# Kernel tuning notes

Hardware: AMD Instinct MI355X
Metric: run time of the kernel (lower is better)

## Reference

```python
import jax, jax.numpy as jnp
import numpy as np

DMODEL = 1024
NHEAD = 16
DHEAD = DMODEL // NHEAD

def _layernorm(x, g, b, eps=1e-5):
    mu = jnp.mean(x, axis=-1, keepdims=True)
    var = jnp.var(x, axis=-1, keepdims=True)
    return (x - mu) * jax.lax.rsqrt(var + eps) * g + b

def setup_inputs() -> dict:
    key = jax.random.key(0)
    ks = jax.random.split(key, 12)
    b, lq, lv, d = 2, 2048, 2048, DMODEL
    s = 1.0 / np.sqrt(d)
    return {
        "q": jax.random.normal(ks[0], (b, lq, d), jnp.float32),
        "k": jax.random.normal(ks[1], (b, lv, d), jnp.float32),
        "v": jax.random.normal(ks[2], (b, lv, d), jnp.float32),
        "qln_g": jnp.ones((d,), jnp.float32),
        "qln_b": jnp.zeros((d,), jnp.float32),
        "kvln_g": jnp.ones((d,), jnp.float32),
        "kvln_b": jnp.zeros((d,), jnp.float32),
        "Wq": jax.random.normal(ks[3], (d, d), jnp.float32) * s,
        "Wk": jax.random.normal(ks[4], (d, d), jnp.float32) * s,
        "Wv": jax.random.normal(ks[5], (d, d), jnp.float32) * s,
        "Wg": jax.random.normal(ks[6], (d, d), jnp.float32) * s,
        "bg": jnp.zeros((d,), jnp.float32),
        "Wo": jax.random.normal(ks[7], (d, d), jnp.float32) * s,
    }

def reference(q, k, v, qln_g, qln_b, kvln_g, kvln_b, Wq, Wk, Wv, Wg, bg, Wo):
    b, lq, d = q.shape
    lv = v.shape[1]
    qn = _layernorm(q, qln_g, qln_b)           # [b, lq, d]
    q_ = qn @ Wq.T
    kk = _layernorm(k, kvln_g, kvln_b) @ Wk.T
    vv = _layernorm(v, kvln_g, kvln_b) @ Wv.T
    qh = q_.reshape(b, lq, NHEAD, DHEAD)       # bqhd
    kh = kk.reshape(b, lv, NHEAD, DHEAD)
    vh = vv.reshape(b, lv, NHEAD, DHEAD)
    scores = jnp.einsum('bqhd,bkhd->bhqk', qh, kh) / np.sqrt(DHEAD)
    attn = jax.nn.softmax(scores, axis=-1)
    y = jnp.einsum('bhqk,bkhd->bqhd', attn, vh).reshape(b, lq, d)
    g = jax.nn.sigmoid(qn @ Wg.T + bg)
    return (y * g) @ Wo.T
```

## Files before the change

### kernel.cpp

```cpp
#include <hip/hip_runtime.h>
#include <hip/hip_bf16.h>

#define DMODEL 1024
#define NHEAD  16
#define DHEAD  64
#define BATCH  2
#define LQ     2048
#define LV     2048
#define ROWS   (BATCH*LQ)
#define WELEMS (DMODEL*DMODEL)
#define BH     (BATCH*NHEAD)

typedef short bf16x8 __attribute__((ext_vector_type(8)));
typedef float f32x4  __attribute__((ext_vector_type(4)));

__device__ __forceinline__ float bf2f(unsigned short s) {
    union { unsigned u; float f; } v; v.u = ((unsigned)s) << 16;
    return v.f;
}
__device__ __forceinline__ unsigned pk_bf(float a, float b) {
    union { __hip_bfloat162 h; unsigned u; } c;
    c.h = __float22bfloat162_rn(make_float2(a, b));
    return c.u;
}

__device__ __forceinline__ void cp16_g2l(const void* g, void* l) {
    __builtin_amdgcn_global_load_lds(
        (const __attribute__((address_space(1))) void*)g,
        (__attribute__((address_space(3))) void*)l,
        16, 0, 0);
}

#define QSCALE (0.125f * 1.4426950408889634f)

#define PREP_WBLK (5 * 256)
#define PREP_NBLK (PREP_WBLK + 3 * ROWS / 4)

__global__ __launch_bounds__(256) void prep_kernel(
    const float* q, const float* k, const float* v,
    const float* qg, const float* qb, const float* kvg, const float* kvb,
    const float* Wq, const float* Wk, const float* Wv, const float* Wg, const float* Wo,
    unsigned short* qn, unsigned short* kn, unsigned short* vn, unsigned short* wb)
{
    int bx = blockIdx.x, tid = threadIdx.x;
    if (bx < PREP_WBLK) {
        int z = bx >> 8;
        const float* srcs[5] = {Wq, Wk, Wv, Wg, Wo};
        size_t base = (size_t)(bx & 255) * 4096;
        const float* s = srcs[z] + base;
        unsigned short* d = wb + (size_t)z * WELEMS + base;
        #pragma unroll
        for (int u = 0; u < 4; ++u) {
            int i = u * 1024 + tid * 4;
            float4 x = *(const float4*)(s + i);
            *(uint2*)(d + i) = make_uint2(pk_bf(x.x, x.y), pk_bf(x.z, x.w));
        }
        return;
    }
    int wave = tid >> 6, lane = tid & 63;
    int gr = (bx - PREP_WBLK) * 4 + wave;
    int tz = gr >> 12, row = gr & 4095;
    const float *x, *gp, *bp; unsigned short* o;
    if      (tz == 0) { x = q; gp = qg;  bp = qb;  o = qn; }
    else if (tz == 1) { x = k; gp = kvg; bp = kvb; o = kn; }
    else              { x = v; gp = kvg; bp = kvb; o = vn; }
    const float* xr = x + (size_t)row * DMODEL;

    float4 xv[4];
    float s = 0.f, sq = 0.f;
    #pragma unroll
    for (int u = 0; u < 4; ++u) {
        xv[u] = *(const float4*)(xr + u * 256 + lane * 4);
        s  += xv[u].x + xv[u].y + xv[u].z + xv[u].w;
        sq += xv[u].x*xv[u].x + xv[u].y*xv[u].y + xv[u].z*xv[u].z + xv[u].w*xv[u].w;
    }
    #pragma unroll
    for (int off = 1; off < 64; off <<= 1) { s += __shfl_xor(s, off); sq += __shfl_xor(sq, off); }
    float mu  = s * (1.0f / DMODEL);
    float var = sq * (1.0f / DMODEL) - mu * mu;
    float inv = rsqrtf(var + 1e-5f);

    unsigned short* orow = o + (size_t)row * DMODEL;
    #pragma unroll
    for (int u = 0; u < 4; ++u) {
        int col = u * 256 + lane * 4;
        float4 gv = *(const float4*)(gp + col);
        float4 bv = *(const float4*)(bp + col);
        float r0 = (xv[u].x - mu) * inv * gv.x + bv.x;
        float r1 = (xv[u].y - mu) * inv * gv.y + bv.y;
        float r2 = (xv[u].z - mu) * inv * gv.z + bv.z;
        float r3 = (xv[u].w - mu) * inv * gv.w + bv.w;
        *(uint2*)(orow + col) = make_uint2(pk_bf(r0, r1), pk_bf(r2, r3));
    }
}

template<int MODE>
__device__ __forceinline__ void gemm256_core(
    const unsigned short* A, const unsigned short* Bw,
    unsigned short* Obf, const float* bias, float scale,
    unsigned short* Al, unsigned short* Bl, int bm, int bn)
{
    int tid  = threadIdx.x;
    int w = tid >> 6, l = tid & 63, quad = l >> 4, L = l & 15;
    int wm = w >> 2, wn = w & 3;

    int c16 = (l & 7) ^ (l >> 3);
    const unsigned short* gAs = A  + (size_t)(bm * 256 + w * 8 + (l >> 3)) * DMODEL + c16 * 8;
    const unsigned short* gBs = Bw + (size_t)(bn * 256 + w * 8 + (l >> 3)) * DMODEL + c16 * 8;
    int dstE = w * 512;

    #define STG_A2(t, ro) do { const unsigned short* s_ = gAs + (size_t)(ro) * DMODEL + (t) * 64; \
        unsigned short* d_ = Al + ((t) & 1) * 16384 + (ro) * 64 + dstE;                           \
        cp16_g2l(s_, d_); cp16_g2l(s_ + 64 * DMODEL, d_ + 4096); } while (0)
    #define STG_B2(t, ro) do { const unsigned short* s_ = gBs + (size_t)(ro) * DMODEL + (t) * 64; \
        unsigned short* d_ = Bl + ((t) & 1) * 16384 + (ro) * 64 + dstE;                           \
        cp16_g2l(s_, d_); cp16_g2l(s_ + 64 * DMODEL, d_ + 4096); } while (0)

    int sw = (L & 7) << 3;
    int o0 = (quad * 8) ^ sw;
    int o1 = (32 + quad * 8) ^ sw;

    f32x4 acc[8][4];
    #pragma unroll
    for (int i = 0; i < 8; ++i)
        #pragma unroll
        for (int j = 0; j < 4; ++j) acc[i][j] = (f32x4){0.f, 0.f, 0.f, 0.f};

    STG_A2(0, 0); STG_A2(0, 128); STG_B2(0, 0); STG_B2(0, 128);
    STG_A2(1, 0); STG_A2(1, 128);
    asm volatile("s_waitcnt vmcnt(4)" ::: "memory");
    __builtin_amdgcn_s_barrier();

    const int NT = DMODEL / 64;
    for (int t = 0; t < NT; ++t) {
        const unsigned short* Ab = Al + (t & 1) * 16384 + wm * 8192;
        const unsigned short* Bb = Bl + (t & 1) * 16384 + wn * 4096;
        bf16x8 b0[4], b1[4], a0[2], a1[2], r0v[6], r1v[6];

        #pragma unroll
        for (int j = 0; j < 4; ++j) {
            b0[j] = *(const bf16x8*)&Bb[(j * 16 + L) * 64 + o0];
            b1[j] = *(const bf16x8*)&Bb[(j * 16 + L) * 64 + o1];
        }
        #pragma unroll
        for (int i2 = 0; i2 < 2; ++i2) {
            a0[i2] = *(const bf16x8*)&Ab[(i2 * 16 + L) * 64 + o0];
            a1[i2] = *(const bf16x8*)&Ab[(i2 * 16 + L) * 64 + o1];
        }
        if (t + 1 < NT) STG_B2(t + 1, 0);
        __builtin_amdgcn_s_barrier();
        __builtin_amdgcn_s_setprio(1);
        #pragma unroll
        for (int i2 = 0; i2 < 2; ++i2)
            #pragma unroll
            for (int j = 0; j < 4; ++j) {
                if (MODE == 3) {
                    acc[i2][j] = __builtin_amdgcn_mfma_f32_16x16x32_bf16(a0[i2], b0[j], acc[i2][j], 0, 0, 0);
                    acc[i2][j] = __builtin_amdgcn_mfma_f32_16x16x32_bf16(a1[i2], b1[j], acc[i2][j], 0, 0, 0);
                } else {
                    acc[i2][j] = __builtin_amdgcn_mfma_f32_16x16x32_bf16(b0[j], a0[i2], acc[i2][j], 0, 0, 0);
                    acc[i2][j] = __builtin_amdgcn_mfma_f32_16x16x32_bf16(b1[j], a1[i2], acc[i2][j], 0, 0, 0);
                }
            }
        __builtin_amdgcn_s_setprio(0);
        __builtin_amdgcn_s_barrier();

        #pragma unroll
        for (int r = 0; r < 6; ++r) {
            r0v[r] = *(const bf16x8*)&Ab[((32 + r * 16) + L) * 64 + o0];
            r1v[r] = *(const bf16x8*)&Ab[((32 + r * 16) + L) * 64 + o1];
        }
        if (t + 1 < NT) STG_B2(t + 1, 128);
        __builtin_amdgcn_s_barrier();
        __builtin_amdgcn_s_setprio(1);
        #pragma unroll
        for (int i2 = 0; i2 < 2; ++i2)
            #pragma unroll
            for (int j = 0; j < 4; ++j) {
                if (MODE == 3) {
                    acc[2 + i2][j] = __builtin_amdgcn_mfma_f32_16x16x32_bf16(r0v[i2], b0[j], acc[2 + i2][j], 0, 0, 0);
                    acc[2 + i2][j] = __builtin_amdgcn_mfma_f32_16x16x32_bf16(r1v[i2], b1[j], acc[2 + i2][j], 0, 0, 0);
                } else {
                    acc[2 + i2][j] = __builtin_amdgcn_mfma_f32_16x16x32_bf16(b0[j], r0v[i2], acc[2 + i2][j], 0, 0, 0);
                    acc[2 + i2][j] = __builtin_amdgcn_mfma_f32_16x16x32_bf16(b1[j], r1v[i2], acc[2 + i2][j], 0, 0, 0);
                }
            }
        __builtin_amdgcn_s_setprio(0);
        asm volatile("s_waitcnt lgkmcnt(0)" ::: "memory");
        __builtin_amdgcn_sched_barrier(0);
        __builtin_amdgcn_s_barrier();

        if (t + 2 < NT) { STG_A2(t + 2, 0); STG_A2(t + 2, 128); }
        __builtin_amdgcn_s_barrier();
        __builtin_amdgcn_s_setprio(1);
        #pragma unroll
        for (int i2 = 0; i2 < 4; ++i2)
            #pragma unroll
            for (int j = 0; j < 4; ++j) {
                if (MODE == 3) {
                    acc[4 + i2][j] = __builtin_amdgcn_mfma_f32_16x16x32_bf16(r0v[2 + i2], b0[j], acc[4 + i2][j], 0, 0, 0);
                    acc[4 + i2][j] = __builtin_amdgcn_mfma_f32_16x16x32_bf16(r1v[2 + i2], b1[j], acc[4 + i2][j], 0, 0, 0);
                } else {
                    acc[4 + i2][j] = __builtin_amdgcn_mfma_f32_16x16x32_bf16(b0[j], r0v[2 + i2], acc[4 + i2][j], 0, 0, 0);
                    acc[4 + i2][j] = __builtin_amdgcn_mfma_f32_16x16x32_bf16(b1[j], r1v[2 + i2], acc[4 + i2][j], 0, 0, 0);
                }
            }
        __builtin_amdgcn_s_setprio(0);
        if (t + 2 < NT) asm volatile("s_waitcnt vmcnt(4)" ::: "memory");
        else            asm volatile("s_waitcnt vmcnt(0)" ::: "memory");
        __builtin_amdgcn_s_barrier();
    }
    #undef STG_A2
    #undef STG_B2

    #pragma unroll
    for (int i = 0; i < 8; ++i) {
        #pragma unroll
        for (int j = 0; j < 4; ++j) {
            f32x4 a = acc[i][j];
            if (MODE == 3) {
                int gcol  = bn * 256 + wn * 64 + j * 16 + L;
                int grow0 = bm * 256 + wm * 128 + i * 16 + quad * 4;
                int b = grow0 >> 11, key0 = grow0 & 2047;
                int h = gcol >> 6,   dd   = gcol & 63;
                uint2 o = make_uint2(pk_bf(a[0], a[1]), pk_bf(a[2], a[3]));
                *(uint2*)&Obf[(((size_t)(b * NHEAD + h) * DHEAD + dd) << 11) + key0] = o;
            } else {
                int grow  = bm * 256 + wm * 128 + i * 16 + L;
                int gcol0 = bn * 256 + wn * 64 + j * 16 + quad * 4;
                size_t idx = (size_t)grow * DMODEL + gcol0;
                if (MODE == 0) {
                    uint2 o = make_uint2(pk_bf(a[0] * scale, a[1] * scale),
                                         pk_bf(a[2] * scale, a[3] * scale));
                    *(uint2*)&Obf[idx] = o;
                } else {
                    float4 bv = *(const float4*)&bias[gcol0];
                    float s0 = 1.0f / (1.0f + __expf(-(a[0] + bv.x)));
                    float s1 = 1.0f / (1.0f + __expf(-(a[1] + bv.y)));
                    float s2 = 1.0f / (1.0f + __expf(-(a[2] + bv.z)));
                    float s3 = 1.0f / (1.0f + __expf(-(a[3] + bv.w)));
                    *(uint2*)&Obf[idx] = make_uint2(pk_bf(s0, s1), pk_bf(s2, s3));
                }
            }
        }
    }
}

__global__ __launch_bounds__(512, 2) void gemm256_kernel(
    const unsigned short* qn, const unsigned short* kn, const unsigned short* vn,
    const unsigned short* wb,
    unsigned short* qs, unsigned short* kkp, unsigned short* vt, unsigned short* gate,
    const float* bg)
{
    __shared__ __align__(16) unsigned short Al[2 * 256 * 64];
    __shared__ __align__(16) unsigned short Bl[2 * 256 * 64];
    int f = blockIdx.x, xcd = f & 7, s = f >> 3;
    int z  = xcd & 3;
    int bm = ((xcd >> 2) << 3) | (s >> 2);
    int bn = s & 3;
    switch (z) {
        case 0:  gemm256_core<0>(qn, wb + 0 * WELEMS, qs,   nullptr, QSCALE, Al, Bl, bm, bn); break;
        case 1:  gemm256_core<0>(kn, wb + 1 * WELEMS, kkp,  nullptr, 1.0f,   Al, Bl, bm, bn); break;
        case 2:  gemm256_core<3>(vn, wb + 2 * WELEMS, vt,   nullptr, 1.0f,   Al, Bl, bm, bn); break;
        default: gemm256_core<1>(qn, wb + 3 * WELEMS, gate, bg,      1.0f,   Al, Bl, bm, bn); break;
    }
}

__device__ __forceinline__ void xcd_map(int& bm, int& bn) {
    int f = blockIdx.y * 8 + blockIdx.x;
    int xcd = f & 7, s = f >> 3;
    bn = s & 7;
    bm = ((s >> 3) << 3) | xcd;
}

__global__ __launch_bounds__(256, 2) void gemm_f32out_kernel(
    const unsigned short* A, const unsigned short* Bw, float* O)
{
    __shared__ __align__(16) unsigned short Al[2 * 128 * 64];
    __shared__ __align__(16) unsigned short Bl[2 * 128 * 64];
    int bm, bn; xcd_map(bm, bn);
    int tid = threadIdx.x;
    int w = tid >> 6, l = tid & 63, quad = l >> 4, L = l & 15;
    int wm = w >> 1, wn = w & 1;

    int c16 = (l & 7) ^ (l >> 3);
    const unsigned short* gAs = A  + (size_t)(bm * 128 + w * 8 + (l >> 3)) * DMODEL + c16 * 8;
    const unsigned short* gBs = Bw + (size_t)(bn * 128 + w * 8 + (l >> 3)) * DMODEL + c16 * 8;
    int dstE = w * 512;

    #define STG4(t, gp, lp) do { const unsigned short* s_ = (gp) + (t) * 64;  \
        unsigned short* d_ = (lp) + ((t) & 1) * 8192 + dstE;                  \
        cp16_g2l(s_,               d_);                                       \
        cp16_g2l(s_ + 32 * DMODEL, d_ + 2048);                                \
        cp16_g2l(s_ + 64 * DMODEL, d_ + 4096);                                \
        cp16_g2l(s_ + 96 * DMODEL, d_ + 6144); } while (0)

    int sw = (L & 7) << 3;
    int o0 = (quad * 8) ^ sw;
    int o1 = (32 + quad * 8) ^ sw;

    f32x4 acc[4][4];
    #pragma unroll
    for (int i = 0; i < 4; ++i)
        #pragma unroll
        for (int j = 0; j < 4; ++j) acc[i][j] = (f32x4){0.f, 0.f, 0.f, 0.f};

    STG4(0, gAs, Al); STG4(0, gBs, Bl);

    const int NT = DMODEL / 64;
    for (int t = 0; t < NT; ++t) {
        if (t + 1 < NT) {
            STG4(t + 1, gAs, Al); STG4(t + 1, gBs, Bl);
            asm volatile("s_waitcnt vmcnt(8)" ::: "memory");
        } else {
            asm volatile("s_waitcnt vmcnt(0)" ::: "memory");
        }
        __builtin_amdgcn_s_barrier();

        const unsigned short* Ab = Al + (t & 1) * 8192 + (wm * 64) * 64;
        const unsigned short* Bb = Bl + (t & 1) * 8192 + (wn * 64) * 64;
        bf16x8 a0[4], a1[4], b0[4], b1[4];
        #pragma unroll
        for (int j = 0; j < 4; ++j) {
            b0[j] = *(const bf16x8*)&Bb[(j * 16 + L) * 64 + o0];
            b1[j] = *(const bf16x8*)&Bb[(j * 16 + L) * 64 + o1];
        }
        #pragma unroll
        for (int i = 0; i < 4; ++i) {
            a0[i] = *(const bf16x8*)&Ab[(i * 16 + L) * 64 + o0];
            a1[i] = *(const bf16x8*)&Ab[(i * 16 + L) * 64 + o1];
        }
        __builtin_amdgcn_s_setprio(1);
        #pragma unroll
        for (int i = 0; i < 4; ++i)
            #pragma unroll
            for (int j = 0; j < 4; ++j) {
                acc[i][j] = __builtin_amdgcn_mfma_f32_16x16x32_bf16(b0[j], a0[i], acc[i][j], 0, 0, 0);
                acc[i][j] = __builtin_amdgcn_mfma_f32_16x16x32_bf16(b1[j], a1[i], acc[i][j], 0, 0, 0);
            }
        __builtin_amdgcn_s_setprio(0);
        __builtin_amdgcn_s_barrier();
    }
    #undef STG4

    #pragma unroll
    for (int i = 0; i < 4; ++i) {
        #pragma unroll
        for (int j = 0; j < 4; ++j) {
            int grow  = bm * 128 + wm * 64 + i * 16 + L;
            int gcol0 = bn * 128 + wn * 64 + j * 16 + quad * 4;
            *(f32x4*)&O[(size_t)grow * DMODEL + gcol0] = acc[i][j];
        }
    }
}

__global__ __launch_bounds__(256, 4) void attn_kernel(
    const unsigned short* qs, const unsigned short* kk, const unsigned short* vt,
    const unsigned short* gate, unsigned short* yg)
{
    __shared__ __align__(16) unsigned short Kl[2 * 64 * 64];
    __shared__ __align__(16) unsigned short Vl[3 * 64 * 64];

    int tid  = threadIdx.x;
    int wave = tid >> 6, lane = tid & 63, quad = lane >> 4, L = lane & 15;

    int f  = blockIdx.y * 32 + blockIdx.x;
    int bh = (f & 7) * 4 + ((f >> 3) & 3);
    int qt = f >> 5;
    int bb = bh >> 4, h = bh & 15;
    int q0 = qt * 64;

    const unsigned short* Qb =
        qs + ((size_t)(bb * LQ + q0 + wave * 16 + L)) * DMODEL + h * DHEAD;
    bf16x8 aq0 = *(const bf16x8*)(Qb + quad * 8);
    bf16x8 aq1 = *(const bf16x8*)(Qb + 32 + quad * 8);

    f32x4 acc[4];
    #pragma unroll
    for (int nt = 0; nt < 4; ++nt) acc[nt] = (f32x4){0.f, 0.f, 0.f, 0.f};
    f32x4 lacc = (f32x4){0.f, 0.f, 0.f, 0.f};
    bf16x8 ones;
    #pragma unroll
    for (int j = 0; j < 8; ++j) ones[j] = (short)0x3F80;

    int rloc = lane >> 3;
    int c16  = (lane & 7) ^ rloc;
    int key0 = (wave & 1) * 32 + (rloc >> 2) * 8 + (wave >> 1) * 4 + (rloc & 3);

    const unsigned short* gK = kk + (size_t)bb * LV * DMODEL + h * DHEAD
                                  + (size_t)key0 * DMODEL + c16 * 8;
    const unsigned short* gV = vt + ((size_t)((bb * NHEAD + h) * DHEAD
                                  + wave * 16 + rloc)) * LV + c16 * 8;
    char* KlB = (char*)Kl;
    char* VlB = (char*)Vl;
    int dst0 = wave * 2048;

    int sl0 = (quad ^ (L & 7)) * 8;

    cp16_g2l(gK,               KlB + dst0);
    cp16_g2l(gK + 16 * DMODEL, KlB + dst0 + 1024);
    cp16_g2l(gV,               VlB + dst0);
    cp16_g2l(gV + 8 * LV,      VlB + dst0 + 1024);
    __syncthreads();
    gK += 64 * DMODEL; gV += 64;
    cp16_g2l(gK,               KlB + 8192 + dst0);
    cp16_g2l(gK + 16 * DMODEL, KlB + 8192 + dst0 + 1024);
    cp16_g2l(gV,               VlB + 8192 + dst0);
    cp16_g2l(gV + 8 * LV,      VlB + 8192 + dst0 + 1024);

    bf16x8 pap0, pap1;

    {
        const unsigned short* Kb = Kl;
        f32x4 zz[4];
        __builtin_amdgcn_s_setprio(1);
        #pragma unroll
        for (int kt = 0; kt < 4; ++kt) {
            bf16x8 bk0 = *(const bf16x8*)&Kb[(kt * 16 + L) * 64 + sl0];
            bf16x8 bk1 = *(const bf16x8*)&Kb[(kt * 16 + L) * 64 + (sl0 ^ 32)];
            f32x4 z = (f32x4){0.f, 0.f, 0.f, 0.f};
            z = __builtin_amdgcn_mfma_f32_16x16x32_bf16(bk0, aq0, z, 0, 0, 0);
            z = __builtin_amdgcn_mfma_f32_16x16x32_bf16(bk1, aq1, z, 0, 0, 0);
            zz[kt] = z;
        }
        __builtin_amdgcn_s_setprio(0);
        union { unsigned u[4]; bf16x8 h; } pa0, pa1;
        pa0.u[0] = pk_bf(__builtin_amdgcn_exp2f(zz[0][0]), __builtin_amdgcn_exp2f(zz[0][1]));
        pa0.u[1] = pk_bf(__builtin_amdgcn_exp2f(zz[0][2]), __builtin_amdgcn_exp2f(zz[0][3]));
        pa0.u[2] = pk_bf(__builtin_amdgcn_exp2f(zz[2][0]), __builtin_amdgcn_exp2f(zz[2][1]));
        pa0.u[3] = pk_bf(__builtin_amdgcn_exp2f(zz[2][2]), __builtin_amdgcn_exp2f(zz[2][3]));
        pa1.u[0] = pk_bf(__builtin_amdgcn_exp2f(zz[1][0]), __builtin_amdgcn_exp2f(zz[1][1]));
        pa1.u[1] = pk_bf(__builtin_amdgcn_exp2f(zz[1][2]), __builtin_amdgcn_exp2f(zz[1][3]));
        pa1.u[2] = pk_bf(__builtin_amdgcn_exp2f(zz[3][0]), __builtin_amdgcn_exp2f(zz[3][1]));
        pa1.u[3] = pk_bf(__builtin_amdgcn_exp2f(zz[3][2]), __builtin_amdgcn_exp2f(zz[3][3]));
        pap0 = pa0.h; pap1 = pa1.h;
    }

    const int NT = LV / 64;
    int vs = 2;
    int vr = 0;
    for (int t = 1; t < NT; ++t) {
        __syncthreads();
        if (t + 1 < NT) {
            gK += 64 * DMODEL; gV += 64;
            int kb = ((t + 1) & 1) * 8192;
            cp16_g2l(gK,               KlB + kb + dst0);
            cp16_g2l(gK + 16 * DMODEL, KlB + kb + dst0 + 1024);
            int vb_ = vs * 8192;
            cp16_g2l(gV,               VlB + vb_ + dst0);
            cp16_g2l(gV + 8 * LV,      VlB + vb_ + dst0 + 1024);
            vs = (vs == 2) ? 0 : vs + 1;
        }
        const unsigned short* Vb = Vl + vr * 4096;
        vr = (vr == 2) ? 0 : vr + 1;
        const unsigned short* Kb = Kl + (t & 1) * 4096;

        bf16x8 vf0[4], vf1[4];
        #pragma unroll
        for (int nt = 0; nt < 4; ++nt) {
            vf0[nt] = *(const bf16x8*)&Vb[(nt * 16 + L) * 64 + sl0];
            vf1[nt] = *(const bf16x8*)&Vb[(nt * 16 + L) * 64 + (sl0 ^ 32)];
        }
        bf16x8 kf0[4], kf1[4];
        #pragma unroll
        for (int kt = 0; kt < 4; ++kt) {
            kf0[kt] = *(const bf16x8*)&Kb[(kt * 16 + L) * 64 + sl0];
            kf1[kt] = *(const bf16x8*)&Kb[(kt * 16 + L) * 64 + (sl0 ^ 32)];
        }

        __builtin_amdgcn_s_setprio(1);
        lacc = __builtin_amdgcn_mfma_f32_16x16x32_bf16(ones, pap0, lacc, 0, 0, 0);
        lacc = __builtin_amdgcn_mfma_f32_16x16x32_bf16(ones, pap1, lacc, 0, 0, 0);
        #pragma unroll
        for (int nt = 0; nt < 4; ++nt) {
            acc[nt] = __builtin_amdgcn_mfma_f32_16x16x32_bf16(vf0[nt], pap0, acc[nt], 0, 0, 0);
            acc[nt] = __builtin_amdgcn_mfma_f32_16x16x32_bf16(vf1[nt], pap1, acc[nt], 0, 0, 0);
        }
        f32x4 zz[4];
        #pragma unroll
        for (int kt = 0; kt < 4; ++kt) {
            f32x4 z = (f32x4){0.f, 0.f, 0.f, 0.f};
            z = __builtin_amdgcn_mfma_f32_16x16x32_bf16(kf0[kt], aq0, z, 0, 0, 0);
            z = __builtin_amdgcn_mfma_f32_16x16x32_bf16(kf1[kt], aq1, z, 0, 0, 0);
            zz[kt] = z;
        }
        __builtin_amdgcn_s_setprio(0);
        union { unsigned u[4]; bf16x8 h; } pa0, pa1;
        pa0.u[0] = pk_bf(__builtin_amdgcn_exp2f(zz[0][0]), __builtin_amdgcn_exp2f(zz[0][1]));
        pa0.u[1] = pk_bf(__builtin_amdgcn_exp2f(zz[0][2]), __builtin_amdgcn_exp2f(zz[0][3]));
        pa0.u[2] = pk_bf(__builtin_amdgcn_exp2f(zz[2][0]), __builtin_amdgcn_exp2f(zz[2][1]));
        pa0.u[3] = pk_bf(__builtin_amdgcn_exp2f(zz[2][2]), __builtin_amdgcn_exp2f(zz[2][3]));
        pa1.u[0] = pk_bf(__builtin_amdgcn_exp2f(zz[1][0]), __builtin_amdgcn_exp2f(zz[1][1]));
        pa1.u[1] = pk_bf(__builtin_amdgcn_exp2f(zz[1][2]), __builtin_amdgcn_exp2f(zz[1][3]));
        pa1.u[2] = pk_bf(__builtin_amdgcn_exp2f(zz[3][0]), __builtin_amdgcn_exp2f(zz[3][1]));
        pa1.u[3] = pk_bf(__builtin_amdgcn_exp2f(zz[3][2]), __builtin_amdgcn_exp2f(zz[3][3]));
        pap0 = pa0.h; pap1 = pa1.h;
    }

    {
        const unsigned short* Vb = Vl + 1 * 4096;
        bf16x8 vf0[4], vf1[4];
        #pragma unroll
        for (int nt = 0; nt < 4; ++nt) {
            vf0[nt] = *(const bf16x8*)&Vb[(nt * 16 + L) * 64 + sl0];
            vf1[nt] = *(const bf16x8*)&Vb[(nt * 16 + L) * 64 + (sl0 ^ 32)];
        }
        lacc = __builtin_amdgcn_mfma_f32_16x16x32_bf16(ones, pap0, lacc, 0, 0, 0);
        lacc = __builtin_amdgcn_mfma_f32_16x16x32_bf16(ones, pap1, lacc, 0, 0, 0);
        #pragma unroll
        for (int nt = 0; nt < 4; ++nt) {
            acc[nt] = __builtin_amdgcn_mfma_f32_16x16x32_bf16(vf0[nt], pap0, acc[nt], 0, 0, 0);
            acc[nt] = __builtin_amdgcn_mfma_f32_16x16x32_bf16(vf1[nt], pap1, acc[nt], 0, 0, 0);
        }
    }

    float inv_l = 1.0f / lacc[0];
    size_t rb = ((size_t)(bb * LQ + q0 + wave * 16 + L)) * DMODEL + h * DHEAD;
    #pragma unroll
    for (int nt = 0; nt < 4; ++nt) {
        size_t idx = rb + nt * 16 + quad * 4;
        ushort4 g = *(const ushort4*)&gate[idx];
        float y0 = acc[nt][0] * inv_l * bf2f(g.x);
        float y1 = acc[nt][1] * inv_l * bf2f(g.y);
        float y2 = acc[nt][2] * inv_l * bf2f(g.z);
        float y3 = acc[nt][3] * inv_l * bf2f(g.w);
        *(uint2*)&yg[idx] = make_uint2(pk_bf(y0, y1), pk_bf(y2, y3));
    }
}

extern "C" void kernel_launch(void* const* d_in, const int* in_sizes, int n_in,
                              void* d_out, int out_size, void* d_ws, size_t ws_size,
                              hipStream_t stream)
{
    const float* q      = (const float*)d_in[0];
    const float* k      = (const float*)d_in[1];
    const float* v      = (const float*)d_in[2];
    const float* qln_g  = (const float*)d_in[3];
    const float* qln_b  = (const float*)d_in[4];
    const float* kvln_g = (const float*)d_in[5];
    const float* kvln_b = (const float*)d_in[6];
    const float* Wq     = (const float*)d_in[7];
    const float* Wk     = (const float*)d_in[8];
    const float* Wv     = (const float*)d_in[9];
    const float* Wg     = (const float*)d_in[10];
    const float* bg     = (const float*)d_in[11];
    const float* Wo     = (const float*)d_in[12];
    float* out = (float*)d_out;

    const size_t T8 = (size_t)ROWS * DMODEL * 2;
    char* ws = (char*)d_ws;
    unsigned short* qn   = (unsigned short*)(ws + 0 * T8);
    unsigned short* kn   = (unsigned short*)(ws + 1 * T8);
    unsigned short* vn   = (unsigned short*)(ws + 2 * T8);
    unsigned short* qs   = (unsigned short*)(ws + 3 * T8);
    unsigned short* kkp  = (unsigned short*)(ws + 4 * T8);
    unsigned short* vt   = (unsigned short*)(ws + 5 * T8);
    unsigned short* gate = (unsigned short*)(ws + 6 * T8);
    unsigned short* yg   = (unsigned short*)(ws + 7 * T8);
    unsigned short* wb   = (unsigned short*)(ws + 8 * T8);

    prep_kernel<<<dim3(PREP_NBLK), 256, 0, stream>>>(
        q, k, v, qln_g, qln_b, kvln_g, kvln_b, Wq, Wk, Wv, Wg, Wo, qn, kn, vn, wb);
    gemm256_kernel<<<dim3(256), 512, 0, stream>>>(
        qn, kn, vn, wb, qs, kkp, vt, gate, bg);
    attn_kernel<<<dim3(32, 32), 256, 0, stream>>>(qs, kkp, vt, gate, yg);
    gemm_f32out_kernel<<<dim3(DMODEL / 128, ROWS / 128), 256, 0, stream>>>(yg, wb + 4 * WELEMS, out);
}
```

Measured before the change: 226.2 us.

## Restructure GEMM main loop into four phases with one-tile-ahead prefetch

Reorganizes the 256x256 bf16 GEMM core so each K-step runs in four MFMA phases, each loading only two A fragments, instead of three phases that preloaded six extra A fragments into registers. Global-to-LDS staging of the next tile is spread as single copies across the phases, and prefetch distance for A drops from two tiles ahead to one. The aim is to cut register pressure and interleave memory traffic more evenly with compute. The cost is more barriers per iteration and less latency hiding for A loads.

```diff
diff --git a/kernel.cpp b/kernel.cpp
--- a/kernel.cpp
+++ b/kernel.cpp
@@ -109,12 +109,9 @@
     const unsigned short* gBs = Bw + (size_t)(bn * 256 + w * 8 + (l >> 3)) * DMODEL + c16 * 8;
     int dstE = w * 512;
 
-    #define STG_A2(t, ro) do { const unsigned short* s_ = gAs + (size_t)(ro) * DMODEL + (t) * 64; \
-        unsigned short* d_ = Al + ((t) & 1) * 16384 + (ro) * 64 + dstE;                           \
-        cp16_g2l(s_, d_); cp16_g2l(s_ + 64 * DMODEL, d_ + 4096); } while (0)
-    #define STG_B2(t, ro) do { const unsigned short* s_ = gBs + (size_t)(ro) * DMODEL + (t) * 64; \
-        unsigned short* d_ = Bl + ((t) & 1) * 16384 + (ro) * 64 + dstE;                           \
-        cp16_g2l(s_, d_); cp16_g2l(s_ + 64 * DMODEL, d_ + 4096); } while (0)
+    #define STG1(t, ro, gp, lp)                                               \
+        cp16_g2l((gp) + (size_t)(ro) * DMODEL + (t) * 64,                     \
+                 (lp) + ((t) & 1) * 16384 + (ro) * 64 + dstE)
 
     int sw = (L & 7) << 3;
     int o0 = (quad * 8) ^ sw;
@@ -126,16 +123,18 @@
         #pragma unroll
         for (int j = 0; j < 4; ++j) acc[i][j] = (f32x4){0.f, 0.f, 0.f, 0.f};
 
-    STG_A2(0, 0); STG_A2(0, 128); STG_B2(0, 0); STG_B2(0, 128);
-    STG_A2(1, 0); STG_A2(1, 128);
-    asm volatile("s_waitcnt vmcnt(4)" ::: "memory");
+    STG1(0,   0, gBs, Bl); STG1(0,  64, gBs, Bl);
+    STG1(0, 128, gBs, Bl); STG1(0, 192, gBs, Bl);
+    STG1(0,   0, gAs, Al); STG1(0, 128, gAs, Al);
+    STG1(0,  64, gAs, Al); STG1(0, 192, gAs, Al);
+    asm volatile("s_waitcnt vmcnt(2)" ::: "memory");
     __builtin_amdgcn_s_barrier();
 
     const int NT = DMODEL / 64;
-    for (int t = 0; t < NT; ++t) {
-        const unsigned short* Ab = Al + (t & 1) * 16384 + wm * 8192;
-        const unsigned short* Bb = Bl + (t & 1) * 16384 + wn * 4096;
-        bf16x8 b0[4], b1[4], a0[2], a1[2], r0v[6], r1v[6];
+    for (int g = 0; g < NT; ++g) {
+        const unsigned short* Ab = Al + (g & 1) * 16384 + wm * 8192;
+        const unsigned short* Bb = Bl + (g & 1) * 16384 + wn * 4096;
+        bf16x8 b0[4], b1[4], a0[2], a1[2];
 
         #pragma unroll
         for (int j = 0; j < 4; ++j) {
@@ -143,75 +142,101 @@
             b1[j] = *(const bf16x8*)&Bb[(j * 16 + L) * 64 + o1];
         }
         #pragma unroll
-        for (int i2 = 0; i2 < 2; ++i2) {
-            a0[i2] = *(const bf16x8*)&Ab[(i2 * 16 + L) * 64 + o0];
-            a1[i2] = *(const bf16x8*)&Ab[(i2 * 16 + L) * 64 + o1];
-        }
-        if (t + 1 < NT) STG_B2(t + 1, 0);
-        __builtin_amdgcn_s_barrier();
-        __builtin_amdgcn_s_setprio(1);
-        #pragma unroll
-        for (int i2 = 0; i2 < 2; ++i2)
+        for (int i = 0; i < 2; ++i) {
+            a0[i] = *(const bf16x8*)&Ab[(i * 16 + L) * 64 + o0];
+            a1[i] = *(const bf16x8*)&Ab[(i * 16 + L) * 64 + o1];
+        }
+        if (g + 1 < NT) { STG1(g + 1, 0, gBs, Bl); STG1(g + 1, 64, gBs, Bl); }
+        __builtin_amdgcn_s_barrier();
+        __builtin_amdgcn_s_setprio(1);
+        #pragma unroll
+        for (int i = 0; i < 2; ++i)
             #pragma unroll
             for (int j = 0; j < 4; ++j) {
                 if (MODE == 3) {
-                    acc[i2][j] = __builtin_amdgcn_mfma_f32_16x16x32_bf16(a0[i2], b0[j], acc[i2][j], 0, 0, 0);
-                    acc[i2][j] = __builtin_amdgcn_mfma_f32_16x16x32_bf16(a1[i2], b1[j], acc[i2][j], 0, 0, 0);
+                    acc[i][j] = __builtin_amdgcn_mfma_f32_16x16x32_bf16(a0[i], b0[j], acc[i][j], 0, 0, 0);
+                    acc[i][j] = __builtin_amdgcn_mfma_f32_16x16x32_bf16(a1[i], b1[j], acc[i][j], 0, 0, 0);
                 } else {
-                    acc[i2][j] = __builtin_amdgcn_mfma_f32_16x16x32_bf16(b0[j], a0[i2], acc[i2][j], 0, 0, 0);
-                    acc[i2][j] = __builtin_amdgcn_mfma_f32_16x16x32_bf16(b1[j], a1[i2], acc[i2][j], 0, 0, 0);
+                    acc[i][j] = __builtin_amdgcn_mfma_f32_16x16x32_bf16(b0[j], a0[i], acc[i][j], 0, 0, 0);
+                    acc[i][j] = __builtin_amdgcn_mfma_f32_16x16x32_bf16(b1[j], a1[i], acc[i][j], 0, 0, 0);
                 }
             }
         __builtin_amdgcn_s_setprio(0);
         __builtin_amdgcn_s_barrier();
 
         #pragma unroll
-        for (int r = 0; r < 6; ++r) {
-            r0v[r] = *(const bf16x8*)&Ab[((32 + r * 16) + L) * 64 + o0];
-            r1v[r] = *(const bf16x8*)&Ab[((32 + r * 16) + L) * 64 + o1];
-        }
-        if (t + 1 < NT) STG_B2(t + 1, 128);
-        __builtin_amdgcn_s_barrier();
-        __builtin_amdgcn_s_setprio(1);
-        #pragma unroll
-        for (int i2 = 0; i2 < 2; ++i2)
+        for (int i = 0; i < 2; ++i) {
+            a0[i] = *(const bf16x8*)&Ab[((2 + i) * 16 + L) * 64 + o0];
+            a1[i] = *(const bf16x8*)&Ab[((2 + i) * 16 + L) * 64 + o1];
+        }
+        if (g + 1 < NT) { STG1(g + 1, 128, gBs, Bl); STG1(g + 1, 192, gBs, Bl); }
+        __builtin_amdgcn_s_barrier();
+        __builtin_amdgcn_s_setprio(1);
+        #pragma unroll
+        for (int i = 0; i < 2; ++i)
             #pragma unroll
             for (int j = 0; j < 4; ++j) {
                 if (MODE == 3) {
-                    acc[2 + i2][j] = __builtin_amdgcn_mfma_f32_16x16x32_bf16(r0v[i2], b0[j], acc[2 + i2][j], 0, 0, 0);
-                    acc[2 + i2][j] = __builtin_amdgcn_mfma_f32_16x16x32_bf16(r1v[i2], b1[j], acc[2 + i2][j], 0, 0, 0);
+                    acc[2 + i][j] = __builtin_amdgcn_mfma_f32_16x16x32_bf16(a0[i], b0[j], acc[2 + i][j], 0, 0, 0);
+                    acc[2 + i][j] = __builtin_amdgcn_mfma_f32_16x16x32_bf16(a1[i], b1[j], acc[2 + i][j], 0, 0, 0);
                 } else {
-                    acc[2 + i2][j] = __builtin_amdgcn_mfma_f32_16x16x32_bf16(b0[j], r0v[i2], acc[2 + i2][j], 0, 0, 0);
-                    acc[2 + i2][j] = __builtin_amdgcn_mfma_f32_16x16x32_bf16(b1[j], r1v[i2], acc[2 + i2][j], 0, 0, 0);
+                    acc[2 + i][j] = __builtin_amdgcn_mfma_f32_16x16x32_bf16(b0[j], a0[i], acc[2 + i][j], 0, 0, 0);
+                    acc[2 + i][j] = __builtin_amdgcn_mfma_f32_16x16x32_bf16(b1[j], a1[i], acc[2 + i][j], 0, 0, 0);
                 }
             }
         __builtin_amdgcn_s_setprio(0);
-        asm volatile("s_waitcnt lgkmcnt(0)" ::: "memory");
-        __builtin_amdgcn_sched_barrier(0);
-        __builtin_amdgcn_s_barrier();
-
-        if (t + 2 < NT) { STG_A2(t + 2, 0); STG_A2(t + 2, 128); }
-        __builtin_amdgcn_s_barrier();
-        __builtin_amdgcn_s_setprio(1);
-        #pragma unroll
-        for (int i2 = 0; i2 < 4; ++i2)
+        if (g + 1 < NT) asm volatile("s_waitcnt vmcnt(4)" ::: "memory");
+        else            asm volatile("s_waitcnt vmcnt(0)" ::: "memory");
+        __builtin_amdgcn_s_barrier();
+
+        #pragma unroll
+        for (int i = 0; i < 2; ++i) {
+            a0[i] = *(const bf16x8*)&Ab[((4 + i) * 16 + L) * 64 + o0];
+            a1[i] = *(const bf16x8*)&Ab[((4 + i) * 16 + L) * 64 + o1];
+        }
+        if (g + 1 < NT) { STG1(g + 1, 0, gAs, Al); STG1(g + 1, 128, gAs, Al); }
+        __builtin_amdgcn_s_barrier();
+        __builtin_amdgcn_s_setprio(1);
+        #pragma unroll
+        for (int i = 0; i < 2; ++i)
             #pragma unroll
             for (int j = 0; j < 4; ++j) {
                 if (MODE == 3) {
-                    acc[4 + i2][j] = __builtin_amdgcn_mfma_f32_16x16x32_bf16(r0v[2 + i2], b0[j], acc[4 + i2][j], 0, 0, 0);
-                    acc[4 + i2][j] = __builtin_amdgcn_mfma_f32_16x16x32_bf16(r1v[2 + i2], b1[j], acc[4 + i2][j], 0, 0, 0);
+                    acc[4 + i][j] = __builtin_amdgcn_mfma_f32_16x16x32_bf16(a0[i], b0[j], acc[4 + i][j], 0, 0, 0);
+                    acc[4 + i][j] = __builtin_amdgcn_mfma_f32_16x16x32_bf16(a1[i], b1[j], acc[4 + i][j], 0, 0, 0);
                 } else {
-                    acc[4 + i2][j] = __builtin_amdgcn_mfma_f32_16x16x32_bf16(b0[j], r0v[2 + i2], acc[4 + i2][j], 0, 0, 0);
-                    acc[4 + i2][j] = __builtin_amdgcn_mfma_f32_16x16x32_bf16(b1[j], r1v[2 + i2], acc[4 + i2][j], 0, 0, 0);
+                    acc[4 + i][j] = __builtin_amdgcn_mfma_f32_16x16x32_bf16(b0[j], a0[i], acc[4 + i][j], 0, 0, 0);
+                    acc[4 + i][j] = __builtin_amdgcn_mfma_f32_16x16x32_bf16(b1[j], a1[i], acc[4 + i][j], 0, 0, 0);
                 }
             }
         __builtin_amdgcn_s_setprio(0);
-        if (t + 2 < NT) asm volatile("s_waitcnt vmcnt(4)" ::: "memory");
-        else            asm volatile("s_waitcnt vmcnt(0)" ::: "memory");
-        __builtin_amdgcn_s_barrier();
-    }
-    #undef STG_A2
-    #undef STG_B2
+        __builtin_amdgcn_s_barrier();
+
+        #pragma unroll
+        for (int i = 0; i < 2; ++i) {
+            a0[i] = *(const bf16x8*)&Ab[((6 + i) * 16 + L) * 64 + o0];
+            a1[i] = *(const bf16x8*)&Ab[((6 + i) * 16 + L) * 64 + o1];
+        }
+        if (g + 1 < NT) { STG1(g + 1, 64, gAs, Al); STG1(g + 1, 192, gAs, Al); }
+        __builtin_amdgcn_s_barrier();
+        __builtin_amdgcn_s_setprio(1);
+        #pragma unroll
+        for (int i = 0; i < 2; ++i)
+            #pragma unroll
+            for (int j = 0; j < 4; ++j) {
+                if (MODE == 3) {
+                    acc[6 + i][j] = __builtin_amdgcn_mfma_f32_16x16x32_bf16(a0[i], b0[j], acc[6 + i][j], 0, 0, 0);
+                    acc[6 + i][j] = __builtin_amdgcn_mfma_f32_16x16x32_bf16(a1[i], b1[j], acc[6 + i][j], 0, 0, 0);
+                } else {
+                    acc[6 + i][j] = __builtin_amdgcn_mfma_f32_16x16x32_bf16(b0[j], a0[i], acc[6 + i][j], 0, 0, 0);
+                    acc[6 + i][j] = __builtin_amdgcn_mfma_f32_16x16x32_bf16(b1[j], a1[i], acc[6 + i][j], 0, 0, 0);
+                }
+            }
+        __builtin_amdgcn_s_setprio(0);
+        if (g + 1 < NT) asm volatile("s_waitcnt vmcnt(2)" ::: "memory");
+        __builtin_amdgcn_s_barrier();
+    }
+    #undef STG1
 
     #pragma unroll
     for (int i = 0; i < 8; ++i) {
```

After: 222.8 us. No clear change (-1.5%).

## Replace 256x256 projection GEMM with shared 128x128 tile core

Applied to the files above, without the earlier changes.

The fused Q/K/V/gate projection kernel moves from 256x256 tiles with 512 threads and a hand-interleaved multi-phase schedule to 128x128 tiles with 256 threads and a simple double-buffered loop. This launches 1024 blocks instead of 256 and changes the XCD block mapping. The output-projection kernel now reuses the same core through a new f32 output mode, removing duplicated code. The change aims for better occupancy and load balance across CUs, at the cost of lower per-block data reuse and more global traffic for the operand tiles.

```diff
diff --git a/kernel.cpp b/kernel.cpp
--- a/kernel.cpp
+++ b/kernel.cpp
@@ -95,141 +95,99 @@
 }
 
 template<int MODE>
-__device__ __forceinline__ void gemm256_core(
+__device__ __forceinline__ void gemm128_core(
     const unsigned short* A, const unsigned short* Bw,
-    unsigned short* Obf, const float* bias, float scale,
+    unsigned short* Obf, float* Of32, const float* bias, float scale,
     unsigned short* Al, unsigned short* Bl, int bm, int bn)
 {
-    int tid  = threadIdx.x;
+    int tid = threadIdx.x;
     int w = tid >> 6, l = tid & 63, quad = l >> 4, L = l & 15;
-    int wm = w >> 2, wn = w & 3;
+    int wm = w >> 1, wn = w & 1;
 
     int c16 = (l & 7) ^ (l >> 3);
-    const unsigned short* gAs = A  + (size_t)(bm * 256 + w * 8 + (l >> 3)) * DMODEL + c16 * 8;
-    const unsigned short* gBs = Bw + (size_t)(bn * 256 + w * 8 + (l >> 3)) * DMODEL + c16 * 8;
+    const unsigned short* gAs = A  + (size_t)(bm * 128 + w * 8 + (l >> 3)) * DMODEL + c16 * 8;
+    const unsigned short* gBs = Bw + (size_t)(bn * 128 + w * 8 + (l >> 3)) * DMODEL + c16 * 8;
     int dstE = w * 512;
 
-    #define STG_A2(t, ro) do { const unsigned short* s_ = gAs + (size_t)(ro) * DMODEL + (t) * 64; \
-        unsigned short* d_ = Al + ((t) & 1) * 16384 + (ro) * 64 + dstE;                           \
-        cp16_g2l(s_, d_); cp16_g2l(s_ + 64 * DMODEL, d_ + 4096); } while (0)
-    #define STG_B2(t, ro) do { const unsigned short* s_ = gBs + (size_t)(ro) * DMODEL + (t) * 64; \
-        unsigned short* d_ = Bl + ((t) & 1) * 16384 + (ro) * 64 + dstE;                           \
-        cp16_g2l(s_, d_); cp16_g2l(s_ + 64 * DMODEL, d_ + 4096); } while (0)
+    #define STG4(t, gp, lp) do { const unsigned short* s_ = (gp) + (t) * 64;  \
+        unsigned short* d_ = (lp) + ((t) & 1) * 8192 + dstE;                  \
+        cp16_g2l(s_,               d_);                                       \
+        cp16_g2l(s_ + 32 * DMODEL, d_ + 2048);                                \
+        cp16_g2l(s_ + 64 * DMODEL, d_ + 4096);                                \
+        cp16_g2l(s_ + 96 * DMODEL, d_ + 6144); } while (0)
 
     int sw = (L & 7) << 3;
     int o0 = (quad * 8) ^ sw;
     int o1 = (32 + quad * 8) ^ sw;
 
-    f32x4 acc[8][4];
-    #pragma unroll
-    for (int i = 0; i < 8; ++i)
+    f32x4 acc[4][4];
+    #pragma unroll
+    for (int i = 0; i < 4; ++i)
         #pragma unroll
         for (int j = 0; j < 4; ++j) acc[i][j] = (f32x4){0.f, 0.f, 0.f, 0.f};
 
-    STG_A2(0, 0); STG_A2(0, 128); STG_B2(0, 0); STG_B2(0, 128);
-    STG_A2(1, 0); STG_A2(1, 128);
-    asm volatile("s_waitcnt vmcnt(4)" ::: "memory");
-    __builtin_amdgcn_s_barrier();
+    STG4(0, gAs, Al); STG4(0, gBs, Bl);
 
     const int NT = DMODEL / 64;
     for (int t = 0; t < NT; ++t) {
-        const unsigned short* Ab = Al + (t & 1) * 16384 + wm * 8192;
-        const unsigned short* Bb = Bl + (t & 1) * 16384 + wn * 4096;
-        bf16x8 b0[4], b1[4], a0[2], a1[2], r0v[6], r1v[6];
-
+        if (t + 1 < NT) {
+            STG4(t + 1, gAs, Al); STG4(t + 1, gBs, Bl);
+            asm volatile("s_waitcnt vmcnt(8)" ::: "memory");
+        } else {
+            asm volatile("s_waitcnt vmcnt(0)" ::: "memory");
+        }
+        __builtin_amdgcn_s_barrier();
+
+        const unsigned short* Ab = Al + (t & 1) * 8192 + (wm * 64) * 64;
+        const unsigned short* Bb = Bl + (t & 1) * 8192 + (wn * 64) * 64;
+        bf16x8 a0[4], a1[4], b0[4], b1[4];
         #pragma unroll
         for (int j = 0; j < 4; ++j) {
             b0[j] = *(const bf16x8*)&Bb[(j * 16 + L) * 64 + o0];
             b1[j] = *(const bf16x8*)&Bb[(j * 16 + L) * 64 + o1];
         }
         #pragma unroll
-        for (int i2 = 0; i2 < 2; ++i2) {
-            a0[i2] = *(const bf16x8*)&Ab[(i2 * 16 + L) * 64 + o0];
-            a1[i2] = *(const bf16x8*)&Ab[(i2 * 16 + L) * 64 + o1];
-        }
-        if (t + 1 < NT) STG_B2(t + 1, 0);
-        __builtin_amdgcn_s_barrier();
+        for (int i = 0; i < 4; ++i) {
+            a0[i] = *(const bf16x8*)&Ab[(i * 16 + L) * 64 + o0];
+            a1[i] = *(const bf16x8*)&Ab[(i * 16 + L) * 64 + o1];
+        }
         __builtin_amdgcn_s_setprio(1);
         #pragma unroll
-        for (int i2 = 0; i2 < 2; ++i2)
+        for (int i = 0; i < 4; ++i)
             #pragma unroll
             for (int j = 0; j < 4; ++j) {
                 if (MODE == 3) {
-                    acc[i2][j] = __builtin_amdgcn_mfma_f32_16x16x32_bf16(a0[i2], b0[j], acc[i2][j], 0, 0, 0);
-                    acc[i2][j] = __builtin_amdgcn_mfma_f32_16x16x32_bf16(a1[i2], b1[j], acc[i2][j], 0, 0, 0);
+                    acc[i][j] = __builtin_amdgcn_mfma_f32_16x16x32_bf16(a0[i], b0[j], acc[i][j], 0, 0, 0);
+                    acc[i][j] = __builtin_amdgcn_mfma_f32_16x16x32_bf16(a1[i], b1[j], acc[i][j], 0, 0, 0);
                 } else {
-                    acc[i2][j] = __builtin_amdgcn_mfma_f32_16x16x32_bf16(b0[j], a0[i2], acc[i2][j], 0, 0, 0);
-                    acc[i2][j] = __builtin_amdgcn_mfma_f32_16x16x32_bf16(b1[j], a1[i2], acc[i2][j], 0, 0, 0);
+                    acc[i][j] = __builtin_amdgcn_mfma_f32_16x16x32_bf16(b0[j], a0[i], acc[i][j], 0, 0, 0);
+                    acc[i][j] = __builtin_amdgcn_mfma_f32_16x16x32_bf16(b1[j], a1[i], acc[i][j], 0, 0, 0);
                 }
             }
         __builtin_amdgcn_s_setprio(0);
         __builtin_amdgcn_s_barrier();
-
-        #pragma unroll
-        for (int r = 0; r < 6; ++r) {
-            r0v[r] = *(const bf16x8*)&Ab[((32 + r * 16) + L) * 64 + o0];
-            r1v[r] = *(const bf16x8*)&Ab[((32 + r * 16) + L) * 64 + o1];
-        }
-        if (t + 1 < NT) STG_B2(t + 1, 128);
-        __builtin_amdgcn_s_barrier();
-        __builtin_amdgcn_s_setprio(1);
-        #pragma unroll
-        for (int i2 = 0; i2 < 2; ++i2)
-            #pragma unroll
-            for (int j = 0; j < 4; ++j) {
-                if (MODE == 3) {
-                    acc[2 + i2][j] = __builtin_amdgcn_mfma_f32_16x16x32_bf16(r0v[i2], b0[j], acc[2 + i2][j], 0, 0, 0);
-                    acc[2 + i2][j] = __builtin_amdgcn_mfma_f32_16x16x32_bf16(r1v[i2], b1[j], acc[2 + i2][j], 0, 0, 0);
-                } else {
-                    acc[2 + i2][j] = __builtin_amdgcn_mfma_f32_16x16x32_bf16(b0[j], r0v[i2], acc[2 + i2][j], 0, 0, 0);
-                    acc[2 + i2][j] = __builtin_amdgcn_mfma_f32_16x16x32_bf16(b1[j], r1v[i2], acc[2 + i2][j], 0, 0, 0);
-                }
-            }
-        __builtin_amdgcn_s_setprio(0);
-        asm volatile("s_waitcnt lgkmcnt(0)" ::: "memory");
-        __builtin_amdgcn_sched_barrier(0);
-        __builtin_amdgcn_s_barrier();
-
-        if (t + 2 < NT) { STG_A2(t + 2, 0); STG_A2(t + 2, 128); }
-        __builtin_amdgcn_s_barrier();
-        __builtin_amdgcn_s_setprio(1);
-        #pragma unroll
-        for (int i2 = 0; i2 < 4; ++i2)
-            #pragma unroll
-            for (int j = 0; j < 4; ++j) {
-                if (MODE == 3) {
-                    acc[4 + i2][j] = __builtin_amdgcn_mfma_f32_16x16x32_bf16(r0v[2 + i2], b0[j], acc[4 + i2][j], 0, 0, 0);
-                    acc[4 + i2][j] = __builtin_amdgcn_mfma_f32_16x16x32_bf16(r1v[2 + i2], b1[j], acc[4 + i2][j], 0, 0, 0);
-                } else {
-                    acc[4 + i2][j] = __builtin_amdgcn_mfma_f32_16x16x32_bf16(b0[j], r0v[2 + i2], acc[4 + i2][j], 0, 0, 0);
-                    acc[4 + i2][j] = __builtin_amdgcn_mfma_f32_16x16x32_bf16(b1[j], r1v[2 + i2], acc[4 + i2][j], 0, 0, 0);
-                }
-            }
-        __builtin_amdgcn_s_setprio(0);
-        if (t + 2 < NT) asm volatile("s_waitcnt vmcnt(4)" ::: "memory");
-        else            asm volatile("s_waitcnt vmcnt(0)" ::: "memory");
-        __builtin_amdgcn_s_barrier();
-    }
-    #undef STG_A2
-    #undef STG_B2
-
-    #pragma unroll
-    for (int i = 0; i < 8; ++i) {
+    }
+    #undef STG4
+
+    #pragma unroll
+    for (int i = 0; i < 4; ++i) {
         #pragma unroll
         for (int j = 0; j < 4; ++j) {
             f32x4 a = acc[i][j];
             if (MODE == 3) {
-                int gcol  = bn * 256 + wn * 64 + j * 16 + L;
-                int grow0 = bm * 256 + wm * 128 + i * 16 + quad * 4;
+                int gcol  = bn * 128 + wn * 64 + j * 16 + L;
+                int grow0 = bm * 128 + wm * 64 + i * 16 + quad * 4;
                 int b = grow0 >> 11, key0 = grow0 & 2047;
                 int h = gcol >> 6,   dd   = gcol & 63;
                 uint2 o = make_uint2(pk_bf(a[0], a[1]), pk_bf(a[2], a[3]));
                 *(uint2*)&Obf[(((size_t)(b * NHEAD + h) * DHEAD + dd) << 11) + key0] = o;
             } else {
-                int grow  = bm * 256 + wm * 128 + i * 16 + L;
-                int gcol0 = bn * 256 + wn * 64 + j * 16 + quad * 4;
+                int grow  = bm * 128 + wm * 64 + i * 16 + L;
+                int gcol0 = bn * 128 + wn * 64 + j * 16 + quad * 4;
                 size_t idx = (size_t)grow * DMODEL + gcol0;
-                if (MODE == 0) {
+                if (MODE == 2) {
+                    *(f32x4*)&Of32[idx] = a;
+                } else if (MODE == 0) {
                     uint2 o = make_uint2(pk_bf(a[0] * scale, a[1] * scale),
                                          pk_bf(a[2] * scale, a[3] * scale));
                     *(uint2*)&Obf[idx] = o;
@@ -246,23 +204,23 @@
     }
 }
 
-__global__ __launch_bounds__(512, 2) void gemm256_kernel(
+__global__ __launch_bounds__(256, 2) void gemm128_kernel(
     const unsigned short* qn, const unsigned short* kn, const unsigned short* vn,
     const unsigned short* wb,
     unsigned short* qs, unsigned short* kkp, unsigned short* vt, unsigned short* gate,
     const float* bg)
 {
-    __shared__ __align__(16) unsigned short Al[2 * 256 * 64];
-    __shared__ __align__(16) unsigned short Bl[2 * 256 * 64];
-    int f = blockIdx.x, xcd = f & 7, s = f >> 3;
-    int z  = xcd & 3;
-    int bm = ((xcd >> 2) << 3) | (s >> 2);
-    int bn = s & 3;
+    __shared__ __align__(16) unsigned short Al[2 * 128 * 64];
+    __shared__ __align__(16) unsigned short Bl[2 * 128 * 64];
+    int f = blockIdx.x, xcd = f & 7, r = f >> 3;
+    int z = r >> 5, s = r & 31;
+    int bm = ((s >> 3) << 3) | xcd;
+    int bn = s & 7;
     switch (z) {
-        case 0:  gemm256_core<0>(qn, wb + 0 * WELEMS, qs,   nullptr, QSCALE, Al, Bl, bm, bn); break;
-        case 1:  gemm256_core<0>(kn, wb + 1 * WELEMS, kkp,  nullptr, 1.0f,   Al, Bl, bm, bn); break;
-        case 2:  gemm256_core<3>(vn, wb + 2 * WELEMS, vt,   nullptr, 1.0f,   Al, Bl, bm, bn); break;
-        default: gemm256_core<1>(qn, wb + 3 * WELEMS, gate, bg,      1.0f,   Al, Bl, bm, bn); break;
+        case 0:  gemm128_core<0>(qn, wb + 0 * WELEMS, qs,   nullptr, nullptr, QSCALE, Al, Bl, bm, bn); break;
+        case 1:  gemm128_core<0>(kn, wb + 1 * WELEMS, kkp,  nullptr, nullptr, 1.0f,   Al, Bl, bm, bn); break;
+        case 2:  gemm128_core<3>(vn, wb + 2 * WELEMS, vt,   nullptr, nullptr, 1.0f,   Al, Bl, bm, bn); break;
+        default: gemm128_core<1>(qn, wb + 3 * WELEMS, gate, nullptr, bg,      1.0f,   Al, Bl, bm, bn); break;
     }
 }
 
@@ -279,79 +237,7 @@
     __shared__ __align__(16) unsigned short Al[2 * 128 * 64];
     __shared__ __align__(16) unsigned short Bl[2 * 128 * 64];
     int bm, bn; xcd_map(bm, bn);
-    int tid = threadIdx.x;
-    int w = tid >> 6, l = tid & 63, quad = l >> 4, L = l & 15;
-    int wm = w >> 1, wn = w & 1;
-
-    int c16 = (l & 7) ^ (l >> 3);
-    const unsigned short* gAs = A  + (size_t)(bm * 128 + w * 8 + (l >> 3)) * DMODEL + c16 * 8;
-    const unsigned short* gBs = Bw + (size_t)(bn * 128 + w * 8 + (l >> 3)) * DMODEL + c16 * 8;
-    int dstE = w * 512;
-
-    #define STG4(t, gp, lp) do { const unsigned short* s_ = (gp) + (t) * 64;  \
-        unsigned short* d_ = (lp) + ((t) & 1) * 8192 + dstE;                  \
-        cp16_g2l(s_,               d_);                                       \
-        cp16_g2l(s_ + 32 * DMODEL, d_ + 2048);                                \
-        cp16_g2l(s_ + 64 * DMODEL, d_ + 4096);                                \
-        cp16_g2l(s_ + 96 * DMODEL, d_ + 6144); } while (0)
-
-    int sw = (L & 7) << 3;
-    int o0 = (quad * 8) ^ sw;
-    int o1 = (32 + quad * 8) ^ sw;
-
-    f32x4 acc[4][4];
-    #pragma unroll
-    for (int i = 0; i < 4; ++i)
-        #pragma unroll
-        for (int j = 0; j < 4; ++j) acc[i][j] = (f32x4){0.f, 0.f, 0.f, 0.f};
-
-    STG4(0, gAs, Al); STG4(0, gBs, Bl);
-
-    const int NT = DMODEL / 64;
-    for (int t = 0; t < NT; ++t) {
-        if (t + 1 < NT) {
-            STG4(t + 1, gAs, Al); STG4(t + 1, gBs, Bl);
-            asm volatile("s_waitcnt vmcnt(8)" ::: "memory");
-        } else {
-            asm volatile("s_waitcnt vmcnt(0)" ::: "memory");
-        }
-        __builtin_amdgcn_s_barrier();
-
-        const unsigned short* Ab = Al + (t & 1) * 8192 + (wm * 64) * 64;
-        const unsigned short* Bb = Bl + (t & 1) * 8192 + (wn * 64) * 64;
-        bf16x8 a0[4], a1[4], b0[4], b1[4];
-        #pragma unroll
-        for (int j = 0; j < 4; ++j) {
-            b0[j] = *(const bf16x8*)&Bb[(j * 16 + L) * 64 + o0];
-            b1[j] = *(const bf16x8*)&Bb[(j * 16 + L) * 64 + o1];
-        }
-        #pragma unroll
-        for (int i = 0; i < 4; ++i) {
-            a0[i] = *(const bf16x8*)&Ab[(i * 16 + L) * 64 + o0];
-            a1[i] = *(const bf16x8*)&Ab[(i * 16 + L) * 64 + o1];
-        }
-        __builtin_amdgcn_s_setprio(1);
-        #pragma unroll
-        for (int i = 0; i < 4; ++i)
-            #pragma unroll
-            for (int j = 0; j < 4; ++j) {
-                acc[i][j] = __builtin_amdgcn_mfma_f32_16x16x32_bf16(b0[j], a0[i], acc[i][j], 0, 0, 0);
-                acc[i][j] = __builtin_amdgcn_mfma_f32_16x16x32_bf16(b1[j], a1[i], acc[i][j], 0, 0, 0);
-            }
-        __builtin_amdgcn_s_setprio(0);
-        __builtin_amdgcn_s_barrier();
-    }
-    #undef STG4
-
-    #pragma unroll
-    for (int i = 0; i < 4; ++i) {
-        #pragma unroll
-        for (int j = 0; j < 4; ++j) {
-            int grow  = bm * 128 + wm * 64 + i * 16 + L;
-            int gcol0 = bn * 128 + wn * 64 + j * 16 + quad * 4;
-            *(f32x4*)&O[(size_t)grow * DMODEL + gcol0] = acc[i][j];
-        }
-    }
+    gemm128_core<2>(A, Bw, nullptr, O, nullptr, 1.0f, Al, Bl, bm, bn);
 }
 
 __global__ __launch_bounds__(256, 4) void attn_kernel(
@@ -561,7 +447,7 @@
 
     prep_kernel<<<dim3(PREP_NBLK), 256, 0, stream>>>(
         q, k, v, qln_g, qln_b, kvln_g, kvln_b, Wq, Wk, Wv, Wg, Wo, qn, kn, vn, wb);
-    gemm256_kernel<<<dim3(256), 512, 0, stream>>>(
+    gemm128_kernel<<<dim3(1024), 256, 0, stream>>>(
         qn, kn, vn, wb, qs, kkp, vt, gate, bg);
     attn_kernel<<<dim3(32, 32), 256, 0, stream>>>(qs, kkp, vt, gate, yg);
     gemm_f32out_kernel<<<dim3(DMODEL / 128, ROWS / 128), 256, 0, stream>>>(yg, wb + 4 * WELEMS, out);
```

After: 234.3 us. 3.6% more time.
